# Optimization experiments

Hardware: AMD Instinct MI355X
Metric: run time of the kernel (lower is better)

Reference implementation:

```python
import jax, jax.numpy as jnp
import numpy as np

B, C, H, W = 32, 512, 56, 56
P = 64  # planes = C / ratio
EPS = 1e-3


def setup_inputs() -> dict:
    key = jax.random.key(0)
    ks = jax.random.split(key, 10)
    return {
        "x": jax.random.normal(ks[0], (B, C, H, W), jnp.float32),
        "wm": jax.random.normal(ks[1], (1, C), jnp.float32) * 0.05,
        "bm": jax.random.normal(ks[2], (1,), jnp.float32) * 0.05,
        "w1": jax.random.normal(ks[3], (P, C), jnp.float32) * 0.05,
        "b1": jax.random.normal(ks[4], (P,), jnp.float32) * 0.05,
        "ln_g": jax.random.normal(ks[5], (P,), jnp.float32) * 0.1 + 1.0,
        "ln_b": jax.random.normal(ks[6], (P,), jnp.float32) * 0.05,
        "w2": jax.random.normal(ks[7], (C, P), jnp.float32) * 0.05,
        "b2": jax.random.normal(ks[8], (C,), jnp.float32) * 0.05,
        "gamma": jax.random.normal(ks[9], (1,), jnp.float32) * 0.1,
    }


def reference(x, wm, bm, w1, b1, ln_g, ln_b, w2, b2, gamma):
    b, c, h, w = x.shape
    xf = x.reshape(b, c, h * w)                       # (B, C, S)
    # attention spatial pool: 1x1 conv mask -> softmax over spatial -> weighted sum
    mask = jnp.einsum('bcs,c->bs', xf, wm[0]) + bm[0]  # (B, S)
    attn = jax.nn.softmax(mask, axis=-1)               # softmax over H*W
    context = jnp.einsum('bcs,bs->bc', xf, attn)       # (B, C)
    # channel_add_conv: 1x1 conv -> LayerNorm([P,1,1], eps=1e-3) -> ReLU -> 1x1 conv
    hid = jnp.einsum('pc,bc->bp', w1, context) + b1    # (B, P)
    mu = hid.mean(axis=-1, keepdims=True)
    var = jnp.mean((hid - mu) ** 2, axis=-1, keepdims=True)
    hid = (hid - mu) / jnp.sqrt(var + EPS) * ln_g + ln_b
    hid = jax.nn.relu(hid)
    add = jnp.einsum('cp,bp->bc', w2, hid) + b2        # (B, C)
    return x + gamma[0] * add[:, :, None, None]
```

## Files before the change

kernel.cpp:

```cpp
#include <hip/hip_runtime.h>

constexpr int kB = 32;
constexpr int kC = 512;
constexpr int kS = 56 * 56;
constexpr int kP = 64;
constexpr float kEps = 1e-3f;

constexpr int kSG = 32;
constexpr int kNG = kS / kSG;
constexpr int kGPB = 2;
static_assert(kS % kSG == 0, "group must divide S");
static_assert(kNG % kGPB == 0, "block must divide groups");

typedef float f4v __attribute__((ext_vector_type(4)));

__global__ __launch_bounds__(128)
void k_pass_a(const float* __restrict__ x, const float* __restrict__ wm,
              float* __restrict__ pc, float* __restrict__ pmz) {
    __shared__ float swm[kC];
    const int t = threadIdx.x;
    swm[t]       = wm[t];
    swm[t + 128] = wm[t + 128];
    swm[t + 256] = wm[t + 256];
    swm[t + 384] = wm[t + 384];
    __syncthreads();

    const int b  = blockIdx.y;
    const int g  = blockIdx.x * kGPB + (t >> 6);
    const int l  = t & 63;
    const int si = l & 7;
    const int cg = l >> 3;
    const int s0 = g * kSG;

    const float* xb = x + (size_t)b * kC * kS + (size_t)cg * kS + s0 + si * 4;

    float m0 = 0.f, m1 = 0.f, m2 = 0.f, m3 = 0.f;
#pragma unroll 8
    for (int k = 0; k < 64; ++k) {
        const f4v v = *(const f4v*)(xb + (size_t)8 * k * kS);
        const float wv = swm[cg + 8 * k];
        m0 += v.x * wv; m1 += v.y * wv; m2 += v.z * wv; m3 += v.w * wv;
    }
#pragma unroll
    for (int off = 8; off <= 32; off <<= 1) {
        m0 += __shfl_xor(m0, off); m1 += __shfl_xor(m1, off);
        m2 += __shfl_xor(m2, off); m3 += __shfl_xor(m3, off);
    }
    float mm = fmaxf(fmaxf(m0, m1), fmaxf(m2, m3));
    mm = fmaxf(mm, __shfl_xor(mm, 1));
    mm = fmaxf(mm, __shfl_xor(mm, 2));
    mm = fmaxf(mm, __shfl_xor(mm, 4));
    const float e0 = expf(m0 - mm), e1 = expf(m1 - mm);
    const float e2 = expf(m2 - mm), e3 = expf(m3 - mm);
    float z = e0 + e1 + e2 + e3;
    z += __shfl_xor(z, 1); z += __shfl_xor(z, 2); z += __shfl_xor(z, 4);
    if (l == 0) {
        pmz[(b * kNG + g) * 2 + 0] = mm;
        pmz[(b * kNG + g) * 2 + 1] = z;
    }

    float* pco = pc + ((size_t)b * kNG + g) * kC;
#pragma unroll 8
    for (int k = 0; k < 64; ++k) {
        const f4v v = *(const f4v*)(xb + (size_t)8 * k * kS);
        float p = v.x * e0 + v.y * e1 + v.z * e2 + v.w * e3;
        p += __shfl_xor(p, 1); p += __shfl_xor(p, 2); p += __shfl_xor(p, 4);
        if (si == 0) pco[cg + 8 * k] = p;
    }
}

__global__ __launch_bounds__(512)
void k_combine_mlp(const float* __restrict__ pc, const float* __restrict__ pmz,
                   const float* __restrict__ w1, const float* __restrict__ b1,
                   const float* __restrict__ ln_g, const float* __restrict__ ln_b,
                   const float* __restrict__ w2, const float* __restrict__ b2,
                   const float* __restrict__ gamma, float* __restrict__ add) {
    const int b = blockIdx.x;
    const int t = threadIdx.x;
    __shared__ float scale[kNG];
    __shared__ float ctx[kC];
    __shared__ float hp[kP][9];
    __shared__ float hid[kP];

    if (t < 64) {
        const float m1 = (t      < kNG) ? pmz[(b * kNG + t     ) * 2] : -INFINITY;
        const float m2 = (t + 64 < kNG) ? pmz[(b * kNG + t + 64) * 2] : -INFINITY;
        float m = fmaxf(m1, m2);
        for (int off = 32; off; off >>= 1) m = fmaxf(m, __shfl_xor(m, off));
        const float e1 = (t      < kNG) ? expf(m1 - m) : 0.f;
        const float e2 = (t + 64 < kNG) ? expf(m2 - m) : 0.f;
        float z = 0.f;
        if (t      < kNG) z += pmz[(b * kNG + t     ) * 2 + 1] * e1;
        if (t + 64 < kNG) z += pmz[(b * kNG + t + 64) * 2 + 1] * e2;
        for (int off = 32; off; off >>= 1) z += __shfl_xor(z, off);
        const float inv = 1.f / z;
        if (t      < kNG) scale[t]      = e1 * inv;
        if (t + 64 < kNG) scale[t + 64] = e2 * inv;
    }
    __syncthreads();

    {
        float acc = 0.f;
        for (int i = 0; i < kNG; ++i)
            acc += pc[((size_t)b * kNG + i) * kC + t] * scale[i];
        ctx[t] = acc;
    }
    __syncthreads();

    {
        const int p = t & 63, k = t >> 6;
        const float* w1p = w1 + p * kC + k * 64;
        const float* cxp = ctx + k * 64;
        float acc = 0.f;
#pragma unroll 8
        for (int i = 0; i < 64; ++i) acc += w1p[i] * cxp[i];
        hp[p][k] = acc;
    }
    __syncthreads();

    if (t < 64) {
        float h = b1[t];
#pragma unroll
        for (int k = 0; k < 8; ++k) h += hp[t][k];
        float mu = h;
        for (int off = 32; off; off >>= 1) mu += __shfl_xor(mu, off);
        mu *= (1.f / kP);
        const float d = h - mu;
        float var = d * d;
        for (int off = 32; off; off >>= 1) var += __shfl_xor(var, off);
        var *= (1.f / kP);
        const float hv = d * rsqrtf(var + kEps) * ln_g[t] + ln_b[t];
        hid[t] = fmaxf(hv, 0.f);
    }
    __syncthreads();

    {
        float a = b2[t];
        const float* w2c = w2 + t * kP;
#pragma unroll
        for (int p = 0; p < kP; ++p) a += w2c[p] * hid[p];
        add[b * kC + t] = gamma[0] * a;
    }
}

constexpr int kOutBlocks = (kB * kC * kS / 4) / (256 * 16);
static_assert(kOutBlocks * 256 * 16 == kB * kC * kS / 4, "exact tiling");

__global__ __launch_bounds__(256)
void k_out(const float* __restrict__ x, const float* __restrict__ addv,
           float* __restrict__ out) {
    const size_t base = (size_t)blockIdx.x * 4096 + threadIdx.x;
#pragma unroll
    for (int j = 0; j < 16; ++j) {
        const size_t i4 = base + (size_t)j * 256;
        const float a = addv[i4 / (kS / 4)];
        const f4v xv = ((const f4v*)x)[i4];
        const f4v o = {xv.x + a, xv.y + a, xv.z + a, xv.w + a};
        ((f4v*)out)[i4] = o;
    }
}

extern "C" void kernel_launch(void* const* d_in, const int* in_sizes, int n_in,
                              void* d_out, int out_size, void* d_ws, size_t ws_size,
                              hipStream_t stream) {
    const float* x     = (const float*)d_in[0];
    const float* wm    = (const float*)d_in[1];
    const float* w1    = (const float*)d_in[3];
    const float* b1    = (const float*)d_in[4];
    const float* ln_g  = (const float*)d_in[5];
    const float* ln_b  = (const float*)d_in[6];
    const float* w2    = (const float*)d_in[7];
    const float* b2    = (const float*)d_in[8];
    const float* gamma = (const float*)d_in[9];
    float* out = (float*)d_out;

    float* ws  = (float*)d_ws;
    float* pc  = ws;
    float* pmz = pc + (size_t)kB * kNG * kC;
    float* add = pmz + (size_t)kB * kNG * 2;

    k_pass_a<<<dim3(kNG / kGPB, kB), kGPB * 64, 0, stream>>>(x, wm, pc, pmz);
    k_combine_mlp<<<kB, 512, 0, stream>>>(pc, pmz, w1, b1, ln_g, ln_b,
                                          w2, b2, gamma, add);
    k_out<<<kOutBlocks, 256, 0, stream>>>(x, add, out);
}
```

Measured before the change: 437.2 us.

## Split channels across two waves and keep x tile in registers for pass A

Pass A now has each block handle one spatial group, with its two wavefronts each covering half of the channels. Each thread holds its 32 float4 x values in registers, so the second pass over x for the weighted context sum reuses them instead of reloading from memory. Partial mask logits are combined across the two waves through shared memory plus one extra barrier. This roughly halves pass A's global reads of x, at the cost of heavy register use (128 VGPRs for the tile) and twice as many blocks.

```diff
diff --git a/kernel.cpp b/kernel.cpp
--- a/kernel.cpp
+++ b/kernel.cpp
@@ -8,44 +8,65 @@
 
 constexpr int kSG = 32;
 constexpr int kNG = kS / kSG;
-constexpr int kGPB = 2;
+constexpr int kCW = kC / 2;
 static_assert(kS % kSG == 0, "group must divide S");
-static_assert(kNG % kGPB == 0, "block must divide groups");
 
 typedef float f4v __attribute__((ext_vector_type(4)));
 
-__global__ __launch_bounds__(128)
+__global__ __launch_bounds__(128, 2)
 void k_pass_a(const float* __restrict__ x, const float* __restrict__ wm,
               float* __restrict__ pc, float* __restrict__ pmz) {
     __shared__ float swm[kC];
-    const int t = threadIdx.x;
+    __shared__ f4v   pmw[2][8];
+
+    const int t  = threadIdx.x;
+    const int w  = t >> 6;
+    const int l  = t & 63;
+    const int si = l & 7;
+    const int cg = l >> 3;
+    const int b  = blockIdx.y;
+    const int g  = blockIdx.x;
+    const int s0 = g * kSG;
+
     swm[t]       = wm[t];
     swm[t + 128] = wm[t + 128];
     swm[t + 256] = wm[t + 256];
     swm[t + 384] = wm[t + 384];
-    __syncthreads();
-
-    const int b  = blockIdx.y;
-    const int g  = blockIdx.x * kGPB + (t >> 6);
-    const int l  = t & 63;
-    const int si = l & 7;
-    const int cg = l >> 3;
-    const int s0 = g * kSG;
-
-    const float* xb = x + (size_t)b * kC * kS + (size_t)cg * kS + s0 + si * 4;
+
+    const float* xb = x + (size_t)b * kC * kS
+                        + (size_t)(w * kCW + cg) * kS + s0 + si * 4;
+
+    f4v xt[32];
+#pragma unroll
+    for (int k = 0; k < 32; ++k)
+        xt[k] = *(const f4v*)(xb + (size_t)(8 * k) * kS);
+
+    __syncthreads();
 
     float m0 = 0.f, m1 = 0.f, m2 = 0.f, m3 = 0.f;
-#pragma unroll 8
-    for (int k = 0; k < 64; ++k) {
-        const f4v v = *(const f4v*)(xb + (size_t)8 * k * kS);
-        const float wv = swm[cg + 8 * k];
-        m0 += v.x * wv; m1 += v.y * wv; m2 += v.z * wv; m3 += v.w * wv;
-    }
+#pragma unroll
+    for (int k = 0; k < 32; ++k) {
+        const float wv = swm[w * kCW + cg + 8 * k];
+        m0 += xt[k].x * wv; m1 += xt[k].y * wv;
+        m2 += xt[k].z * wv; m3 += xt[k].w * wv;
+    }
+
+#pragma unroll
+    for (int k = 0; k < 32; ++k) asm volatile("" : "+v"(xt[k]));
+
 #pragma unroll
     for (int off = 8; off <= 32; off <<= 1) {
         m0 += __shfl_xor(m0, off); m1 += __shfl_xor(m1, off);
         m2 += __shfl_xor(m2, off); m3 += __shfl_xor(m3, off);
     }
+
+    if (l < 8) pmw[w][si] = (f4v){m0, m1, m2, m3};
+    __syncthreads();
+    {
+        const f4v o = pmw[w ^ 1][si];
+        m0 += o.x; m1 += o.y; m2 += o.z; m3 += o.w;
+    }
+
     float mm = fmaxf(fmaxf(m0, m1), fmaxf(m2, m3));
     mm = fmaxf(mm, __shfl_xor(mm, 1));
     mm = fmaxf(mm, __shfl_xor(mm, 2));
@@ -54,18 +75,17 @@
     const float e2 = expf(m2 - mm), e3 = expf(m3 - mm);
     float z = e0 + e1 + e2 + e3;
     z += __shfl_xor(z, 1); z += __shfl_xor(z, 2); z += __shfl_xor(z, 4);
-    if (l == 0) {
+    if (t == 0) {
         pmz[(b * kNG + g) * 2 + 0] = mm;
         pmz[(b * kNG + g) * 2 + 1] = z;
     }
 
-    float* pco = pc + ((size_t)b * kNG + g) * kC;
-#pragma unroll 8
-    for (int k = 0; k < 64; ++k) {
-        const f4v v = *(const f4v*)(xb + (size_t)8 * k * kS);
-        float p = v.x * e0 + v.y * e1 + v.z * e2 + v.w * e3;
+    float* pco = pc + ((size_t)b * kNG + g) * kC + w * kCW;
+#pragma unroll
+    for (int k = 0; k < 32; ++k) {
+        float p = xt[k].x * e0 + xt[k].y * e1 + xt[k].z * e2 + xt[k].w * e3;
         p += __shfl_xor(p, 1); p += __shfl_xor(p, 2); p += __shfl_xor(p, 4);
-        if (si == 0) pco[cg + 8 * k] = p;
+        if (si == 0) pco[8 * k + cg] = p;
     }
 }
 
@@ -179,7 +199,7 @@
     float* pmz = pc + (size_t)kB * kNG * kC;
     float* add = pmz + (size_t)kB * kNG * 2;
 
-    k_pass_a<<<dim3(kNG / kGPB, kB), kGPB * 64, 0, stream>>>(x, wm, pc, pmz);
+    k_pass_a<<<dim3(kNG, kB), 128, 0, stream>>>(x, wm, pc, pmz);
     k_combine_mlp<<<kB, 512, 0, stream>>>(pc, pmz, w1, b1, ln_g, ln_b,
                                           w2, b2, gamma, add);
     k_out<<<kOutBlocks, 256, 0, stream>>>(x, add, out);
```

Measured after the change: 413.9 us. 5.3% less time.
